# Kernel optimization log

Hardware: AMD Instinct MI355X
Metric: run time of the kernel (lower is better)

## Reference

```python
import jax, jax.numpy as jnp
import numpy as np

N = 100000  # nodes
E = 1600000  # edges


def gcn_conv(x, W, b, src, dst, n_nodes):
    """PyG-style GCNConv: add self-loops, symmetric norm, linear, scatter-add, bias."""
    h = x @ W  # [N, F_out]
    loop = jnp.arange(n_nodes, dtype=src.dtype)
    s = jnp.concatenate([src, loop])  # source nodes (messages flow src -> dst)
    d = jnp.concatenate([dst, loop])
    deg = jax.ops.segment_sum(jnp.ones_like(d, dtype=h.dtype), d, num_segments=n_nodes)
    dinv = jnp.where(deg > 0, jax.lax.rsqrt(deg), 0.0)
    norm = dinv[s] * dinv[d]  # [E+N]
    msgs = h[s] * norm[:, None]  # [E+N, F_out] -- dominant memory traffic
    out = jax.ops.segment_sum(msgs, d, num_segments=n_nodes)
    return out + b


def setup_inputs() -> dict:
    key = jax.random.key(0)
    k1, k2, k3, k4 = jax.random.split(key, 4)
    x = jax.random.normal(k1, (N, 128), dtype=jnp.float32)
    edge_index = jax.random.randint(k2, (2, E), 0, N, dtype=jnp.int32)
    W1 = jax.random.normal(k3, (128, 64), dtype=jnp.float32) * (1.0 / np.sqrt(128))
    b1 = jnp.zeros((64,), dtype=jnp.float32)
    W2 = jax.random.normal(k4, (64, 16), dtype=jnp.float32) * (1.0 / np.sqrt(64))
    b2 = jnp.zeros((16,), dtype=jnp.float32)
    return {"x": x, "edge_index": edge_index, "W1": W1, "b1": b1, "W2": W2, "b2": b2}


def reference(x, edge_index, W1, b1, W2, b2):
    src, dst = edge_index[0], edge_index[1]
    h = gcn_conv(x, W1, b1, src, dst, N)
    h = jax.nn.leaky_relu(h, negative_slope=0.2)
    # dropout is identity in eval mode
    h = gcn_conv(h, W2, b2, src, dst, N)
    return jax.nn.log_softmax(h, axis=-1)
```

## Files before the change

### kernel.cpp

```cpp
#include <hip/hip_runtime.h>
#include <math.h>


#define CHUNK 8192
#define BSHIFT 9
#define BMASK 511
#define CAP 9216

typedef __bf16 bf16x8 __attribute__((ext_vector_type(8)));
typedef float f32x4 __attribute__((ext_vector_type(4)));

__device__ __forceinline__ unsigned f2b(float f) {
  unsigned u = __float_as_uint(f);
  return (u + 0x7FFF + ((u >> 16) & 1)) >> 16;
}

__global__ void binit_kernel(int* __restrict__ gbcursor, int nbc,
                             unsigned* __restrict__ h1s, int n) {
  int b = blockIdx.x * 256 + threadIdx.x;
  if (b < nbc) gbcursor[b] = b * CAP;
  if (blockIdx.x == 0 && threadIdx.x < 32) h1s[(size_t)n * 32 + threadIdx.x] = 0u;
}

__global__ __launch_bounds__(256) void scatterA_kernel(const int* __restrict__ src,
                                                       const int* __restrict__ dst,
                                                       int E, int nbc,
                                                       int* __restrict__ gbcursor,
                                                       int* __restrict__ tmp) {
  __shared__ int hist[256];
  __shared__ int segcur[256];
  int tid = threadIdx.x;
  int estart = blockIdx.x * CHUNK;
  int eend = min(E, estart + CHUNK);
  hist[tid] = 0;
  __syncthreads();
  for (int i = estart + tid; i < eend; i += 256)
    atomicAdd(&hist[dst[i] >> BSHIFT], 1);
  __syncthreads();
  if (tid < nbc) {
    int c = hist[tid];
    segcur[tid] = c ? atomicAdd(&gbcursor[tid], c) : 0;
  }
  __syncthreads();
  for (int i = estart + tid; i < eend; i += 256) {
    int d = dst[i];
    int b = d >> BSHIFT;
    int pos = atomicAdd(&segcur[b], 1);
    if (pos < (b + 1) * CAP)
      tmp[pos] = (src[i] << BSHIFT) | (d & BMASK);
  }
}

__global__ __launch_bounds__(256) void csrbuild_kernel(const int* __restrict__ tmp,
                                                       const int* __restrict__ gbcursor,
                                                       int n, int* __restrict__ row_start,
                                                       int* __restrict__ degs,
                                                       float* __restrict__ dinv,
                                                       int* __restrict__ csr) {
  __shared__ int nh[512];
  __shared__ int sp[256];
  __shared__ int lcur[512];
  int b = blockIdx.x, tid = threadIdx.x;
  int base = b * CAP;
  int count = min(gbcursor[b] - base, CAP);
  nh[tid] = 0; nh[tid + 256] = 0;
  __syncthreads();
  for (int i = tid; i < count; i += 256) atomicAdd(&nh[tmp[base + i] & BMASK], 1);
  __syncthreads();
  int d0 = nh[2 * tid], d1 = nh[2 * tid + 1];
  int s = d0 + d1;
  sp[tid] = s;
  __syncthreads();
  for (int off = 1; off < 256; off <<= 1) {
    int a = sp[tid];
    int bb = (tid >= off) ? sp[tid - off] : 0;
    __syncthreads();
    sp[tid] = a + bb;
    __syncthreads();
  }
  int pp = sp[tid] - s;
  int e0a = base + pp;
  int e0b = e0a + d0;
  lcur[2 * tid] = e0a;
  lcur[2 * tid + 1] = e0b;
  int vb = b << BSHIFT;
  int va = vb + 2 * tid;
  if (va < n) {
    row_start[va] = e0a; degs[va] = d0;
    dinv[va] = rsqrtf((float)(d0 + 1));
  }
  if (va + 1 < n) {
    row_start[va + 1] = e0b; degs[va + 1] = d1;
    dinv[va + 1] = rsqrtf((float)(d1 + 1));
  }
  __syncthreads();
  for (int i = tid; i < count; i += 256) {
    int val = tmp[base + i];
    int pos = atomicAdd(&lcur[val & BMASK], 1);
    csr[pos] = val >> BSHIFT;
  }
}

__global__ __launch_bounds__(256, 4) void gemm1_kernel(const float* __restrict__ x,
                                                       const float* __restrict__ W1,
                                                       const float* __restrict__ dinv,
                                                       unsigned* __restrict__ h1s, int n) {
  __shared__ unsigned lds_u[64 * 68 * 2];
  unsigned* xs = lds_u;
  unsigned* wt = lds_u + 64 * 68;
  int tid = threadIdx.x;
  int vb = blockIdx.x * 64;
  int nrows = min(64, n - vb);

  const float4* xg = (const float4*)(x + (size_t)vb * 128);
#pragma unroll
  for (int it = 0; it < 8; ++it) {
    int idx = it * 256 + tid;
    int r = idx >> 5, c2 = idx & 31;
    float4 vv = make_float4(0.f, 0.f, 0.f, 0.f);
    if (r < nrows) vv = xg[idx];
    xs[r * 68 + c2 * 2] = (f2b(vv.y) << 16) | f2b(vv.x);
    xs[r * 68 + c2 * 2 + 1] = (f2b(vv.w) << 16) | f2b(vv.z);
  }
  unsigned short* wt16 = (unsigned short*)wt;
  const float4* wg = (const float4*)W1;
#pragma unroll
  for (int it = 0; it < 8; ++it) {
    int idx = it * 256 + tid;
    int k = idx >> 4, n0 = (idx & 15) * 4;
    float4 wv = wg[idx];
    wt16[(n0 + 0) * 136 + k] = (unsigned short)f2b(wv.x);
    wt16[(n0 + 1) * 136 + k] = (unsigned short)f2b(wv.y);
    wt16[(n0 + 2) * 136 + k] = (unsigned short)f2b(wv.z);
    wt16[(n0 + 3) * 136 + k] = (unsigned short)f2b(wv.w);
  }
  __syncthreads();

  int lane = tid & 63, wid = tid >> 6;
  int m16 = lane & 15, quad = lane >> 4;
  const unsigned* xp = xs + (wid * 16 + m16) * 68 + quad * 4;
  const unsigned* wp = wt + m16 * 68 + quad * 4;
  f32x4 acc[4] = {};
#pragma unroll
  for (int ks = 0; ks < 4; ++ks) {
    bf16x8 a = *(const bf16x8*)(xp + ks * 16);
#pragma unroll
    for (int nt = 0; nt < 4; ++nt) {
      bf16x8 b = *(const bf16x8*)(wp + nt * 16 * 68 + ks * 16);
      acc[nt] = __builtin_amdgcn_mfma_f32_16x16x32_bf16(a, b, acc[nt], 0, 0, 0);
    }
  }
  int rbase = vb + wid * 16 + quad * 4;
  float dvv[4];
#pragma unroll
  for (int reg = 0; reg < 4; ++reg) {
    int row = rbase + reg;
    dvv[reg] = (row < n) ? dinv[row] : 0.f;
  }
  unsigned short* h16 = (unsigned short*)h1s;
#pragma unroll
  for (int nt = 0; nt < 4; ++nt) {
    int col = nt * 16 + m16;
#pragma unroll
    for (int reg = 0; reg < 4; ++reg) {
      int row = rbase + reg;
      if (row < n)
        h16[(size_t)row * 64 + col] = (unsigned short)f2b(dvv[reg] * acc[nt][reg]);
    }
  }
}

struct f2 { float x, y; };
__device__ __forceinline__ void addu(f2& a, unsigned u) {
  a.x += __uint_as_float(u << 16);
  a.y += __uint_as_float(u & 0xFFFF0000u);
}

__global__ __launch_bounds__(256) void agg1_kernel(const uint4* __restrict__ h1s4,
                                                   const float* __restrict__ dinv,
                                                   const int* __restrict__ row_start,
                                                   const int* __restrict__ degs,
                                                   const int* __restrict__ csr,
                                                   const float* __restrict__ b1,
                                                   const float* __restrict__ W2,
                                                   unsigned* __restrict__ t, int n) {
  __shared__ float W2s[64 * 17];
  __shared__ float b1s[64];
  __shared__ float a_s[4][64];
  for (int i = threadIdx.x; i < 1024; i += 256)
    W2s[(i >> 4) * 17 + (i & 15)] = W2[i];
  if (threadIdx.x < 64) b1s[threadIdx.x] = b1[threadIdx.x];
  if (blockIdx.x == 0 && threadIdx.x < 8) t[(size_t)n * 8 + threadIdx.x] = 0u;
  __syncthreads();

  int wave = threadIdx.x >> 6, lane = threadIdx.x & 63;
  int e = lane >> 3, c = lane & 7;
  int j = lane & 15, fb = (lane >> 4) << 4;

  for (int vbase = blockIdx.x * 4; vbase < n; vbase += gridDim.x * 4) {
    int v = vbase + wave;
    bool valid = (v < n);
    int e0 = 0, e1 = 0;
    float dv = 0.f;
    if (valid) { e0 = row_start[v]; e1 = e0 + degs[v]; dv = dinv[v]; }

    f2 a0[4], a1[4];
#pragma unroll
    for (int k = 0; k < 4; ++k) { a0[k] = {0.f, 0.f}; a1[k] = {0.f, 0.f}; }
    {
      int s = (valid && e == 0) ? v : n;
      uint4 g = h1s4[(size_t)s * 8 + c];
      addu(a0[0], g.x); addu(a0[1], g.y); addu(a0[2], g.z); addu(a0[3], g.w);
    }
    int i = e0;
    while (i + 8 < e1) {
      int i1 = i + 8 + e;
      int s0 = csr[i + e];
      int s1v = csr[i1];
      int s1 = (i1 < e1) ? s1v : n;
      uint4 g0 = h1s4[(size_t)s0 * 8 + c];
      uint4 g1 = h1s4[(size_t)s1 * 8 + c];
      addu(a0[0], g0.x); addu(a0[1], g0.y); addu(a0[2], g0.z); addu(a0[3], g0.w);
      addu(a1[0], g1.x); addu(a1[1], g1.y); addu(a1[2], g1.z); addu(a1[3], g1.w);
      i += 16;
    }
    if (i < e1) {
      int i0 = i + e;
      int sv = csr[i0];
      int s = (i0 < e1) ? sv : n;
      uint4 g = h1s4[(size_t)s * 8 + c];
      addu(a0[0], g.x); addu(a0[1], g.y); addu(a0[2], g.z); addu(a0[3], g.w);
    }
#pragma unroll
    for (int k = 0; k < 4; ++k) { a0[k].x += a1[k].x; a0[k].y += a1[k].y; }
#pragma unroll
    for (int m = 8; m <= 32; m <<= 1) {
#pragma unroll
      for (int k = 0; k < 4; ++k) {
        a0[k].x += __shfl_xor(a0[k].x, m, 64);
        a0[k].y += __shfl_xor(a0[k].y, m, 64);
      }
    }
    if (lane < 8) {
#pragma unroll
      for (int k = 0; k < 4; ++k) {
        float z0 = fmaf(dv, a0[k].x, b1s[8 * lane + 2 * k]);
        float z1 = fmaf(dv, a0[k].y, b1s[8 * lane + 2 * k + 1]);
        a_s[wave][8 * lane + 2 * k] = fmaxf(z0, 0.2f * z0);
        a_s[wave][8 * lane + 2 * k + 1] = fmaxf(z1, 0.2f * z1);
      }
    }
    __threadfence_block();
    float p = 0.f;
#pragma unroll
    for (int q = 0; q < 16; ++q)
      p = fmaf(a_s[wave][fb + q], W2s[(fb + q) * 17 + j], p);
    p += __shfl_xor(p, 16, 64);
    p += __shfl_xor(p, 32, 64);
    float pv = dv * p;
    float po = __shfl_xor(pv, 1, 64);
    if (valid && lane < 16 && !(lane & 1))
      t[(size_t)v * 8 + (lane >> 1)] = (f2b(po) << 16) | f2b(pv);
    __threadfence_block();
  }
}

__global__ __launch_bounds__(256) void agg2_kernel(const uint4* __restrict__ t4,
                                                   const float* __restrict__ dinv,
                                                   const int* __restrict__ row_start,
                                                   const int* __restrict__ degs,
                                                   const int* __restrict__ csr,
                                                   const float* __restrict__ b2,
                                                   float* __restrict__ out, int n) {
  int idx = blockIdx.x * 256 + threadIdx.x;
  int v = idx >> 4;
  if (v >= n) return;
  int sub = threadIdx.x & 15;
  int e = sub >> 1, c = sub & 1;
  float dv = dinv[v];
  int e0 = row_start[v], e1 = e0 + degs[v];
  f2 A0[4], A1[4];
#pragma unroll
  for (int k = 0; k < 4; ++k) { A0[k] = {0.f, 0.f}; A1[k] = {0.f, 0.f}; }
  {
    int s = (e == 0) ? v : n;
    uint4 g = t4[(size_t)s * 2 + c];
    addu(A0[0], g.x); addu(A0[1], g.y); addu(A0[2], g.z); addu(A0[3], g.w);
  }
  int i = e0;
  while (i + 8 < e1) {
    int i1 = i + 8 + e;
    int s0 = csr[i + e];
    int s1v = csr[i1];
    int s1 = (i1 < e1) ? s1v : n;
    uint4 g0 = t4[(size_t)s0 * 2 + c];
    uint4 g1 = t4[(size_t)s1 * 2 + c];
    addu(A0[0], g0.x); addu(A0[1], g0.y); addu(A0[2], g0.z); addu(A0[3], g0.w);
    addu(A1[0], g1.x); addu(A1[1], g1.y); addu(A1[2], g1.z); addu(A1[3], g1.w);
    i += 16;
  }
  if (i < e1) {
    int i0 = i + e;
    int sv = csr[i0];
    int s = (i0 < e1) ? sv : n;
    uint4 g = t4[(size_t)s * 2 + c];
    addu(A0[0], g.x); addu(A0[1], g.y); addu(A0[2], g.z); addu(A0[3], g.w);
  }
#pragma unroll
  for (int k = 0; k < 4; ++k) { A0[k].x += A1[k].x; A0[k].y += A1[k].y; }
#pragma unroll
  for (int m = 2; m <= 8; m <<= 1) {
#pragma unroll
    for (int k = 0; k < 4; ++k) {
      A0[k].x += __shfl_xor(A0[k].x, m, 64);
      A0[k].y += __shfl_xor(A0[k].y, m, 64);
    }
  }
  float4 bb0 = ((const float4*)b2)[c * 2];
  float4 bb1 = ((const float4*)b2)[c * 2 + 1];
  float z[8];
  z[0] = fmaf(dv, A0[0].x, bb0.x); z[1] = fmaf(dv, A0[0].y, bb0.y);
  z[2] = fmaf(dv, A0[1].x, bb0.z); z[3] = fmaf(dv, A0[1].y, bb0.w);
  z[4] = fmaf(dv, A0[2].x, bb1.x); z[5] = fmaf(dv, A0[2].y, bb1.y);
  z[6] = fmaf(dv, A0[3].x, bb1.z); z[7] = fmaf(dv, A0[3].y, bb1.w);
  float mx = z[0];
#pragma unroll
  for (int q = 1; q < 8; ++q) mx = fmaxf(mx, z[q]);
  mx = fmaxf(mx, __shfl_xor(mx, 1, 64));
  float ss = 0.f;
#pragma unroll
  for (int q = 0; q < 8; ++q) ss += expf(z[q] - mx);
  ss += __shfl_xor(ss, 1, 64);
  float lg = mx + logf(ss);
  if (e == 0) {
    float4 r0 = make_float4(z[0] - lg, z[1] - lg, z[2] - lg, z[3] - lg);
    float4 r1 = make_float4(z[4] - lg, z[5] - lg, z[6] - lg, z[7] - lg);
    float4* o = (float4*)out + (size_t)v * 4 + c * 2;
    o[0] = r0;
    o[1] = r1;
  }
}

extern "C" void kernel_launch(void* const* d_in, const int* in_sizes, int n_in,
                              void* d_out, int out_size, void* d_ws, size_t ws_size,
                              hipStream_t stream) {
  const float* x = (const float*)d_in[0];
  const int* edge_index = (const int*)d_in[1];
  const float* W1 = (const float*)d_in[2];
  const float* b1 = (const float*)d_in[3];
  const float* W2 = (const float*)d_in[4];
  const float* b2 = (const float*)d_in[5];
  float* out = (float*)d_out;

  int N_ = in_sizes[0] / 128;
  int E_ = in_sizes[1] / 2;
  const int* src = edge_index;
  const int* dst = edge_index + E_;
  int NBc = (N_ + BMASK) >> BSHIFT;

  char* ws = (char*)d_ws;
  size_t off = 0;
  auto take = [&](size_t bytes) {
    void* p = ws + off;
    off += (bytes + 255) & ~(size_t)255;
    return p;
  };
  unsigned* h1s = (unsigned*)take(((size_t)N_ + 1) * 32 * 4);
  size_t t_bytes = ((size_t)N_ + 1) * 8 * 4, tmp_bytes = (size_t)NBc * CAP * 4;
  void* t_union = take(t_bytes > tmp_bytes ? t_bytes : tmp_bytes);
  unsigned* t = (unsigned*)t_union;
  int* tmp = (int*)t_union;
  float* dinv = (float*)take((size_t)N_ * 4);
  int* degs = (int*)take((size_t)N_ * 4);
  int* row_start = (int*)take(((size_t)N_ + 1) * 4);
  int* csr = (int*)take(((size_t)NBc * CAP + 16) * 4);
  int* gbcursor = (int*)take((size_t)NBc * 4);
  (void)ws_size;

  binit_kernel<<<(NBc + 255) / 256, 256, 0, stream>>>(gbcursor, NBc, h1s, N_);
  scatterA_kernel<<<(E_ + CHUNK - 1) / CHUNK, 256, 0, stream>>>(src, dst, E_, NBc,
                                                                gbcursor, tmp);
  csrbuild_kernel<<<NBc, 256, 0, stream>>>(tmp, gbcursor, N_, row_start, degs,
                                           dinv, csr);
  gemm1_kernel<<<(N_ + 63) / 64, 256, 0, stream>>>(x, W1, dinv, h1s, N_);
  agg1_kernel<<<2048, 256, 0, stream>>>((const uint4*)h1s, dinv, row_start, degs,
                                        csr, b1, W2, t, N_);
  agg2_kernel<<<(N_ * 16 + 255) / 256, 256, 0, stream>>>((const uint4*)t, dinv,
                                                         row_start, degs, csr,
                                                         b2, out, N_);
}
```

Measured before the change: 237.7 us.

## Process two nodes per wavefront in layer-1 aggregation with half-wave gathers

The layer-1 aggregation kernel now assigns each half-wavefront (32 lanes) to its own node, so one wave handles two nodes per iteration. Each half gathers 4 edges per load step and loops under a wave-wide any-lane condition. The goal is to cut idle lanes and shuffle-reduction stages for nodes with moderate degree (about 16 neighbours). The bf16 high-half unpack also drops the mask, which adds a small low-bit error to the odd features, and the block-level fences are removed. Some lanes may spin on empty iterations when the two nodes' degrees differ.

```diff
diff --git a/kernel.cpp b/kernel.cpp
--- a/kernel.cpp
+++ b/kernel.cpp
@@ -173,7 +173,10 @@
 struct f2 { float x, y; };
 __device__ __forceinline__ void addu(f2& a, unsigned u) {
   a.x += __uint_as_float(u << 16);
-  a.y += __uint_as_float(u & 0xFFFF0000u);
+  a.y += __uint_as_float(u);
+}
+__device__ __forceinline__ void addu4(f2* a, uint4 g) {
+  addu(a[0], g.x); addu(a[1], g.y); addu(a[2], g.z); addu(a[3], g.w);
 }
 
 __global__ __launch_bounds__(256) void agg1_kernel(const uint4* __restrict__ h1s4,
@@ -186,7 +189,7 @@
                                                    unsigned* __restrict__ t, int n) {
   __shared__ float W2s[64 * 17];
   __shared__ float b1s[64];
-  __shared__ float a_s[4][64];
+  __shared__ float a_s[4][2][64];
   for (int i = threadIdx.x; i < 1024; i += 256)
     W2s[(i >> 4) * 17 + (i & 15)] = W2[i];
   if (threadIdx.x < 64) b1s[threadIdx.x] = b1[threadIdx.x];
@@ -194,74 +197,70 @@
   __syncthreads();
 
   int wave = threadIdx.x >> 6, lane = threadIdx.x & 63;
-  int e = lane >> 3, c = lane & 7;
-  int j = lane & 15, fb = (lane >> 4) << 4;
-
-  for (int vbase = blockIdx.x * 4; vbase < n; vbase += gridDim.x * 4) {
-    int v = vbase + wave;
+  int half = lane >> 5, sub = lane & 31;
+  int e = sub >> 3, c = sub & 7;
+  int j = sub & 15, grp = (sub >> 4) & 1;
+
+  for (int vbase = blockIdx.x * 8; vbase < n; vbase += gridDim.x * 8) {
+    int v = vbase + wave * 2 + half;
     bool valid = (v < n);
-    int e0 = 0, e1 = 0;
-    float dv = 0.f;
-    if (valid) { e0 = row_start[v]; e1 = e0 + degs[v]; dv = dinv[v]; }
-
-    f2 a0[4], a1[4];
-#pragma unroll
-    for (int k = 0; k < 4; ++k) { a0[k] = {0.f, 0.f}; a1[k] = {0.f, 0.f}; }
+    int vc = valid ? v : 0;
+    int i = row_start[vc];
+    int e1 = i + (valid ? degs[vc] : 0);
+    float dv = valid ? dinv[vc] : 0.f;
+
+    f2 a0[4];
+#pragma unroll
+    for (int k = 0; k < 4; ++k) a0[k] = {0.f, 0.f};
     {
-      int s = (valid && e == 0) ? v : n;
-      uint4 g = h1s4[(size_t)s * 8 + c];
-      addu(a0[0], g.x); addu(a0[1], g.y); addu(a0[2], g.z); addu(a0[3], g.w);
-    }
-    int i = e0;
-    while (i + 8 < e1) {
-      int i1 = i + 8 + e;
-      int s0 = csr[i + e];
+      int s = (valid && sub < 8) ? v : n;
+      addu4(a0, h1s4[(size_t)s * 8 + c]);
+    }
+    while (__any(i < e1)) {
+      int i0 = i + e, i1 = i + 4 + e;
+      int s0v = csr[i0];
       int s1v = csr[i1];
+      int s0 = (i0 < e1) ? s0v : n;
       int s1 = (i1 < e1) ? s1v : n;
       uint4 g0 = h1s4[(size_t)s0 * 8 + c];
       uint4 g1 = h1s4[(size_t)s1 * 8 + c];
-      addu(a0[0], g0.x); addu(a0[1], g0.y); addu(a0[2], g0.z); addu(a0[3], g0.w);
-      addu(a1[0], g1.x); addu(a1[1], g1.y); addu(a1[2], g1.z); addu(a1[3], g1.w);
-      i += 16;
-    }
-    if (i < e1) {
-      int i0 = i + e;
-      int sv = csr[i0];
-      int s = (i0 < e1) ? sv : n;
-      uint4 g = h1s4[(size_t)s * 8 + c];
-      addu(a0[0], g.x); addu(a0[1], g.y); addu(a0[2], g.z); addu(a0[3], g.w);
-    }
-#pragma unroll
-    for (int k = 0; k < 4; ++k) { a0[k].x += a1[k].x; a0[k].y += a1[k].y; }
-#pragma unroll
-    for (int m = 8; m <= 32; m <<= 1) {
+      addu4(a0, g0);
+      addu4(a0, g1);
+      i += 8;
+    }
+#pragma unroll
+    for (int m = 8; m <= 16; m <<= 1) {
 #pragma unroll
       for (int k = 0; k < 4; ++k) {
         a0[k].x += __shfl_xor(a0[k].x, m, 64);
         a0[k].y += __shfl_xor(a0[k].y, m, 64);
       }
     }
-    if (lane < 8) {
+    if (sub < 8) {
 #pragma unroll
       for (int k = 0; k < 4; ++k) {
-        float z0 = fmaf(dv, a0[k].x, b1s[8 * lane + 2 * k]);
-        float z1 = fmaf(dv, a0[k].y, b1s[8 * lane + 2 * k + 1]);
-        a_s[wave][8 * lane + 2 * k] = fmaxf(z0, 0.2f * z0);
-        a_s[wave][8 * lane + 2 * k + 1] = fmaxf(z1, 0.2f * z1);
+        float z0 = fmaf(dv, a0[k].x, b1s[8 * sub + 2 * k]);
+        float z1 = fmaf(dv, a0[k].y, b1s[8 * sub + 2 * k + 1]);
+        a_s[wave][half][8 * sub + 2 * k] = fmaxf(z0, 0.2f * z0);
+        a_s[wave][half][8 * sub + 2 * k + 1] = fmaxf(z1, 0.2f * z1);
       }
     }
-    __threadfence_block();
     float p = 0.f;
 #pragma unroll
-    for (int q = 0; q < 16; ++q)
-      p = fmaf(a_s[wave][fb + q], W2s[(fb + q) * 17 + j], p);
+    for (int q = 0; q < 16; ++q) {
+      int f = grp * 16 + q;
+      p = fmaf(a_s[wave][half][f], W2s[f * 17 + j], p);
+    }
+#pragma unroll
+    for (int q = 0; q < 16; ++q) {
+      int f = 32 + grp * 16 + q;
+      p = fmaf(a_s[wave][half][f], W2s[f * 17 + j], p);
+    }
     p += __shfl_xor(p, 16, 64);
-    p += __shfl_xor(p, 32, 64);
     float pv = dv * p;
     float po = __shfl_xor(pv, 1, 64);
-    if (valid && lane < 16 && !(lane & 1))
-      t[(size_t)v * 8 + (lane >> 1)] = (f2b(po) << 16) | f2b(pv);
-    __threadfence_block();
+    if (valid && sub < 16 && !(sub & 1))
+      t[(size_t)v * 8 + (sub >> 1)] = (f2b(po) << 16) | f2b(pv);
   }
 }
 
@@ -284,8 +283,7 @@
   for (int k = 0; k < 4; ++k) { A0[k] = {0.f, 0.f}; A1[k] = {0.f, 0.f}; }
   {
     int s = (e == 0) ? v : n;
-    uint4 g = t4[(size_t)s * 2 + c];
-    addu(A0[0], g.x); addu(A0[1], g.y); addu(A0[2], g.z); addu(A0[3], g.w);
+    addu4(A0, t4[(size_t)s * 2 + c]);
   }
   int i = e0;
   while (i + 8 < e1) {
@@ -295,16 +293,15 @@
     int s1 = (i1 < e1) ? s1v : n;
     uint4 g0 = t4[(size_t)s0 * 2 + c];
     uint4 g1 = t4[(size_t)s1 * 2 + c];
-    addu(A0[0], g0.x); addu(A0[1], g0.y); addu(A0[2], g0.z); addu(A0[3], g0.w);
-    addu(A1[0], g1.x); addu(A1[1], g1.y); addu(A1[2], g1.z); addu(A1[3], g1.w);
+    addu4(A0, g0);
+    addu4(A1, g1);
     i += 16;
   }
   if (i < e1) {
     int i0 = i + e;
     int sv = csr[i0];
     int s = (i0 < e1) ? sv : n;
-    uint4 g = t4[(size_t)s * 2 + c];
-    addu(A0[0], g.x); addu(A0[1], g.y); addu(A0[2], g.z); addu(A0[3], g.w);
+    addu4(A0, t4[(size_t)s * 2 + c]);
   }
 #pragma unroll
   for (int k = 0; k < 4; ++k) { A0[k].x += A1[k].x; A0[k].y += A1[k].y; }
```

After: 227.7 us. -4.2%, faster.
